# Optimization experiments

Measured on AMD Instinct MI355X. Metric: run time of the kernel, lower is better.

The kernel has to match this reference:

```python
import jax, jax.numpy as jnp
import numpy as np

P = 0.8
EPS = 1e-6


def setup_inputs() -> dict:
    key = jax.random.key(0)
    k1, k2 = jax.random.split(key)
    N, C = 8192, 2048
    logits = jax.random.normal(k1, (N, C), dtype=jnp.float32)
    labels = jax.random.randint(k2, (N,), 0, C, dtype=jnp.int64)
    return {"logits": logits, "labels": labels}


def reference(logits, labels):
    N, C = logits.shape
    # targets: one-hot class indicators, [N, C]
    targets = jax.nn.one_hot(labels, C, dtype=logits.dtype)
    # class counts (first-call behavior of the stateful module): sum over batch + 1
    class_counts = targets.sum(axis=0) + 1.0  # [C]
    # seesaw mitigation factor s[i, j] = (n_j / n_i)^p if n_i > n_j else 1
    ratio = class_counts[None, :] / class_counts[:, None]  # [C, C]
    s = jnp.where(class_counts[:, None] > class_counts[None, :], ratio ** P, 1.0)
    # stable exp
    logits = logits - logits.max(axis=-1, keepdims=True)
    e = jnp.exp(logits)  # [N, C]
    # denominator[n, i] = sum_j (1 - t[n,j]) * s[i,j] * e[n,j] + e[n,i]
    # == ((1 - t) * e) @ s.T + e  -- GEMM form of the O(N*C*C) broadcast-sum
    denom = jnp.einsum('nj,ij->ni', (1.0 - targets) * e, s) + e
    sigma = e / (denom + EPS)
    loss = (-targets * jnp.log(sigma + EPS)).sum(axis=-1)  # [N]
    return loss.mean()
```

## Files before the change

kernel.cpp:

```cpp
#include <hip/hip_runtime.h>
#include <math.h>

#define NROWS 8192
#define NCLS  2048
#define NBLK  512
#define NTHR  512
#define LOG2E 1.44269504088896340736f
#define EPS   1e-6f


__global__ __launch_bounds__(512, 4) void seesaw_rows_k(
        const float* __restrict__ logits,
        const int*   __restrict__ labels,
        float*       __restrict__ part) {
    __shared__ __align__(16) int   cnt[NCLS];
    __shared__ __align__(16) float w[NCLS];
    __shared__ float red[8];

    const int t    = threadIdx.x;
    const int lane = t & 63;
    const int wid  = t >> 6;

    const int n0 = blockIdx.x * 16 + wid * 2;
    const int n1 = n0 + 1;

    const int4* lab4 = reinterpret_cast<const int4*>(labels);
    int4 L0 = lab4[t];
    int4 L1 = lab4[t + 512];
    int4 L2 = lab4[t + 1024];
    int4 L3 = lab4[t + 1536];

    const int y0 = labels[n0];
    const int y1 = labels[n1];

    const float4* r0 = reinterpret_cast<const float4*>(logits + (size_t)n0 * NCLS);
    const float4* r1 = reinterpret_cast<const float4*>(logits + (size_t)n1 * NCLS);
    float4 va[8], vb[8];
    #pragma unroll
    for (int k = 0; k < 8; ++k) va[k] = r0[k * 64 + lane];
    #pragma unroll
    for (int k = 0; k < 8; ++k) vb[k] = r1[k * 64 + lane];

    const float ylog0 = logits[(size_t)n0 * NCLS + y0];
    const float ylog1 = logits[(size_t)n1 * NCLS + y1];

    #pragma unroll
    for (int j = t; j < NCLS; j += NTHR) cnt[j] = 0;
    asm volatile("s_waitcnt lgkmcnt(0)" ::: "memory");
    __builtin_amdgcn_s_barrier();
    asm volatile("" ::: "memory");

    atomicAdd(&cnt[L0.x], 1); atomicAdd(&cnt[L0.y], 1);
    atomicAdd(&cnt[L0.z], 1); atomicAdd(&cnt[L0.w], 1);
    atomicAdd(&cnt[L1.x], 1); atomicAdd(&cnt[L1.y], 1);
    atomicAdd(&cnt[L1.z], 1); atomicAdd(&cnt[L1.w], 1);
    atomicAdd(&cnt[L2.x], 1); atomicAdd(&cnt[L2.y], 1);
    atomicAdd(&cnt[L2.z], 1); atomicAdd(&cnt[L2.w], 1);
    atomicAdd(&cnt[L3.x], 1); atomicAdd(&cnt[L3.y], 1);
    atomicAdd(&cnt[L3.z], 1); atomicAdd(&cnt[L3.w], 1);
    asm volatile("s_waitcnt lgkmcnt(0)" ::: "memory");
    __builtin_amdgcn_s_barrier();
    asm volatile("" ::: "memory");

    #pragma unroll
    for (int j = t; j < NCLS; j += NTHR) w[j] = 0.8f * log2f((float)(cnt[j] + 1));
    asm volatile("s_waitcnt lgkmcnt(0)" ::: "memory");
    __builtin_amdgcn_s_barrier();
    asm volatile("" ::: "memory");

    const float4* wl4 = reinterpret_cast<const float4*>(w);
    const float wy0 = w[y0];
    const float wy1 = w[y1];

    float s0 = 0.0f, s1 = 0.0f;
    #pragma unroll
    for (int k = 0; k < 8; ++k) {
        float4 wv = wl4[k * 64 + lane];
        s0 += exp2f(fmaf(va[k].x, LOG2E, fminf(wv.x - wy0, 0.0f)));
        s0 += exp2f(fmaf(va[k].y, LOG2E, fminf(wv.y - wy0, 0.0f)));
        s0 += exp2f(fmaf(va[k].z, LOG2E, fminf(wv.z - wy0, 0.0f)));
        s0 += exp2f(fmaf(va[k].w, LOG2E, fminf(wv.w - wy0, 0.0f)));
        s1 += exp2f(fmaf(vb[k].x, LOG2E, fminf(wv.x - wy1, 0.0f)));
        s1 += exp2f(fmaf(vb[k].y, LOG2E, fminf(wv.y - wy1, 0.0f)));
        s1 += exp2f(fmaf(vb[k].z, LOG2E, fminf(wv.z - wy1, 0.0f)));
        s1 += exp2f(fmaf(vb[k].w, LOG2E, fminf(wv.w - wy1, 0.0f)));
    }
    #pragma unroll
    for (int off = 32; off; off >>= 1) {
        s0 += __shfl_xor(s0, off, 64);
        s1 += __shfl_xor(s1, off, 64);
    }

    if (lane == 0) {
        float ey0 = exp2f(ylog0 * LOG2E);
        float ey1 = exp2f(ylog1 * LOG2E);
        float l0 = -logf(ey0 / (s0 + EPS) + EPS);
        float l1 = -logf(ey1 / (s1 + EPS) + EPS);
        red[wid] = l0 + l1;
    }
    __syncthreads();
    if (t == 0) {
        float bs = ((red[0] + red[1]) + (red[2] + red[3])) +
                   ((red[4] + red[5]) + (red[6] + red[7]));
        part[blockIdx.x] = bs;
    }
}

__global__ __launch_bounds__(256) void finalize_k(
        const float* __restrict__ part, float* __restrict__ out) {
    const int t = threadIdx.x, lane = t & 63, wid = t >> 6;
    float s = part[t] + part[t + 256];
    #pragma unroll
    for (int off = 32; off; off >>= 1) s += __shfl_xor(s, off, 64);
    __shared__ float red[4];
    if (lane == 0) red[wid] = s;
    __syncthreads();
    if (t == 0) out[0] = ((red[0] + red[1]) + (red[2] + red[3])) / (float)NROWS;
}

extern "C" void kernel_launch(void* const* d_in, const int* in_sizes, int n_in,
                              void* d_out, int out_size, void* d_ws, size_t ws_size,
                              hipStream_t stream) {
    const float* logits = (const float*)d_in[0];
    const int*   labels = (const int*)d_in[1];
    float* out  = (float*)d_out;
    float* part = (float*)d_ws;

    seesaw_rows_k<<<NBLK, NTHR, 0, stream>>>(logits, labels, part);
    finalize_k<<<1, 256, 0, stream>>>(part, out);
}
```

Baseline: 20.44 us.

## Fuse finalize into main kernel via two-level last-block atomic reduction

Drops the separate finalize kernel. Each block publishes its partial sum, and per-group atomic counters elect a last block that reduces 32 partials; a second counter elects the final block, which writes the mean. A memset of the counters is added before the launch. The second row's loads are deferred until after the histogram phase to lower register pressure, and the exp accumulations are split into two independent chains each. This trades a kernel launch for a memset node plus atomics.

```diff
diff --git a/kernel.cpp b/kernel.cpp
--- a/kernel.cpp
+++ b/kernel.cpp
@@ -9,19 +9,24 @@
 #define EPS   1e-6f
 
 
-__global__ __launch_bounds__(512, 4) void seesaw_rows_k(
+__global__ __launch_bounds__(512, 4) void seesaw_all_k(
         const float* __restrict__ logits,
         const int*   __restrict__ labels,
-        float*       __restrict__ part) {
+        char*        __restrict__ wsb,
+        float*       __restrict__ out) {
     __shared__ __align__(16) int   cnt[NCLS];
     __shared__ __align__(16) float w[NCLS];
     __shared__ float red[8];
 
+    float* part = (float*)wsb;
+    float* gsum = (float*)(wsb + 2048);
+
     const int t    = threadIdx.x;
     const int lane = t & 63;
     const int wid  = t >> 6;
+    const int bid  = blockIdx.x;
 
-    const int n0 = blockIdx.x * 16 + wid * 2;
+    const int n0 = bid * 16 + wid * 2;
     const int n1 = n0 + 1;
 
     const int4* lab4 = reinterpret_cast<const int4*>(labels);
@@ -34,18 +39,14 @@
     const int y1 = labels[n1];
 
     const float4* r0 = reinterpret_cast<const float4*>(logits + (size_t)n0 * NCLS);
-    const float4* r1 = reinterpret_cast<const float4*>(logits + (size_t)n1 * NCLS);
-    float4 va[8], vb[8];
+    float4 va[8];
     #pragma unroll
     for (int k = 0; k < 8; ++k) va[k] = r0[k * 64 + lane];
-    #pragma unroll
-    for (int k = 0; k < 8; ++k) vb[k] = r1[k * 64 + lane];
 
     const float ylog0 = logits[(size_t)n0 * NCLS + y0];
     const float ylog1 = logits[(size_t)n1 * NCLS + y1];
 
-    #pragma unroll
-    for (int j = t; j < NCLS; j += NTHR) cnt[j] = 0;
+    reinterpret_cast<int4*>(cnt)[t] = make_int4(0, 0, 0, 0);
     asm volatile("s_waitcnt lgkmcnt(0)" ::: "memory");
     __builtin_amdgcn_s_barrier();
     asm volatile("" ::: "memory");
@@ -68,23 +69,36 @@
     __builtin_amdgcn_s_barrier();
     asm volatile("" ::: "memory");
 
+    const float4* r1 = reinterpret_cast<const float4*>(logits + (size_t)n1 * NCLS);
+    float4 vb[8];
+    #pragma unroll
+    for (int k = 0; k < 8; ++k) vb[k] = r1[k * 64 + lane];
+
     const float4* wl4 = reinterpret_cast<const float4*>(w);
     const float wy0 = w[y0];
     const float wy1 = w[y1];
 
-    float s0 = 0.0f, s1 = 0.0f;
+    float s0a = 0.0f, s0b = 0.0f;
     #pragma unroll
     for (int k = 0; k < 8; ++k) {
         float4 wv = wl4[k * 64 + lane];
-        s0 += exp2f(fmaf(va[k].x, LOG2E, fminf(wv.x - wy0, 0.0f)));
-        s0 += exp2f(fmaf(va[k].y, LOG2E, fminf(wv.y - wy0, 0.0f)));
-        s0 += exp2f(fmaf(va[k].z, LOG2E, fminf(wv.z - wy0, 0.0f)));
-        s0 += exp2f(fmaf(va[k].w, LOG2E, fminf(wv.w - wy0, 0.0f)));
-        s1 += exp2f(fmaf(vb[k].x, LOG2E, fminf(wv.x - wy1, 0.0f)));
-        s1 += exp2f(fmaf(vb[k].y, LOG2E, fminf(wv.y - wy1, 0.0f)));
-        s1 += exp2f(fmaf(vb[k].z, LOG2E, fminf(wv.z - wy1, 0.0f)));
-        s1 += exp2f(fmaf(vb[k].w, LOG2E, fminf(wv.w - wy1, 0.0f)));
+        s0a += exp2f(fmaf(va[k].x, LOG2E, fminf(wv.x - wy0, 0.0f)));
+        s0b += exp2f(fmaf(va[k].y, LOG2E, fminf(wv.y - wy0, 0.0f)));
+        s0a += exp2f(fmaf(va[k].z, LOG2E, fminf(wv.z - wy0, 0.0f)));
+        s0b += exp2f(fmaf(va[k].w, LOG2E, fminf(wv.w - wy0, 0.0f)));
     }
+    float s1a = 0.0f, s1b = 0.0f;
+    #pragma unroll
+    for (int k = 0; k < 8; ++k) {
+        float4 wv = wl4[k * 64 + lane];
+        s1a += exp2f(fmaf(vb[k].x, LOG2E, fminf(wv.x - wy1, 0.0f)));
+        s1b += exp2f(fmaf(vb[k].y, LOG2E, fminf(wv.y - wy1, 0.0f)));
+        s1a += exp2f(fmaf(vb[k].z, LOG2E, fminf(wv.z - wy1, 0.0f)));
+        s1b += exp2f(fmaf(vb[k].w, LOG2E, fminf(wv.w - wy1, 0.0f)));
+    }
+
+    float s0 = s0a + s0b;
+    float s1 = s1a + s1b;
     #pragma unroll
     for (int off = 32; off; off >>= 1) {
         s0 += __shfl_xor(s0, off, 64);
@@ -99,23 +113,51 @@
         red[wid] = l0 + l1;
     }
     __syncthreads();
+
     if (t == 0) {
         float bs = ((red[0] + red[1]) + (red[2] + red[3])) +
                    ((red[4] + red[5]) + (red[6] + red[7]));
-        part[blockIdx.x] = bs;
+        __hip_atomic_store(&part[bid], bs, __ATOMIC_RELAXED,
+                           __HIP_MEMORY_SCOPE_AGENT);
     }
-}
-
-__global__ __launch_bounds__(256) void finalize_k(
-        const float* __restrict__ part, float* __restrict__ out) {
-    const int t = threadIdx.x, lane = t & 63, wid = t >> 6;
-    float s = part[t] + part[t + 256];
-    #pragma unroll
-    for (int off = 32; off; off >>= 1) s += __shfl_xor(s, off, 64);
-    __shared__ float red[4];
-    if (lane == 0) red[wid] = s;
-    __syncthreads();
-    if (t == 0) out[0] = ((red[0] + red[1]) + (red[2] + red[3])) / (float)NROWS;
+    if (t < 64) {
+        const int g = bid >> 5;
+        int rc = -1;
+        if (t == 0) {
+            unsigned* gc = (unsigned*)(wsb + 4096 + (size_t)g * 64);
+            rc = (int)__hip_atomic_fetch_add(gc, 1u, __ATOMIC_ACQ_REL,
+                                             __HIP_MEMORY_SCOPE_AGENT);
+        }
+        rc = __shfl(rc, 0, 64);
+        if (rc == 31) {
+            __threadfence();
+            float p = 0.0f;
+            if (t < 32)
+                p = __hip_atomic_load(&part[g * 32 + t], __ATOMIC_RELAXED,
+                                      __HIP_MEMORY_SCOPE_AGENT);
+            #pragma unroll
+            for (int off = 16; off; off >>= 1) p += __shfl_xor(p, off, 32);
+            int rc2 = -1;
+            if (t == 0) {
+                __hip_atomic_store(&gsum[g], p, __ATOMIC_RELAXED,
+                                   __HIP_MEMORY_SCOPE_AGENT);
+                unsigned* fc = (unsigned*)(wsb + 5120);
+                rc2 = (int)__hip_atomic_fetch_add(fc, 1u, __ATOMIC_ACQ_REL,
+                                                  __HIP_MEMORY_SCOPE_AGENT);
+            }
+            rc2 = __shfl(rc2, 0, 64);
+            if (rc2 == 15) {
+                __threadfence();
+                float q = 0.0f;
+                if (t < 16)
+                    q = __hip_atomic_load(&gsum[t], __ATOMIC_RELAXED,
+                                          __HIP_MEMORY_SCOPE_AGENT);
+                #pragma unroll
+                for (int off = 8; off; off >>= 1) q += __shfl_xor(q, off, 32);
+                if (t == 0) out[0] = q / (float)NROWS;
+            }
+        }
+    }
 }
 
 extern "C" void kernel_launch(void* const* d_in, const int* in_sizes, int n_in,
@@ -123,9 +165,9 @@
                               hipStream_t stream) {
     const float* logits = (const float*)d_in[0];
     const int*   labels = (const int*)d_in[1];
-    float* out  = (float*)d_out;
-    float* part = (float*)d_ws;
+    float* out = (float*)d_out;
+    char*  wsb = (char*)d_ws;
 
-    seesaw_rows_k<<<NBLK, NTHR, 0, stream>>>(logits, labels, part);
-    finalize_k<<<1, 256, 0, stream>>>(part, out);
+    hipMemsetAsync(wsb + 4096, 0, 1088, stream);
+    seesaw_all_k<<<NBLK, NTHR, 0, stream>>>(logits, labels, wsb, out);
 }
```

Result: slower. 37.12 us (+81.6%).

## Process one row per wave and double the block count

Applied to the files above, without the earlier changes.

Each wave now handles one row instead of two, so the grid doubles to 1024 blocks and the launch bound rises to 6 blocks per CU, lowering register pressure to allow more resident waves. The sum is split into two accumulators for more instruction-level parallelism, the count zeroing uses one vector store, and the finalize kernel reads partials as float4. The cost is that each block rebuilds the full label histogram, so that redundant per-block work doubles.

```diff
diff --git a/kernel.cpp b/kernel.cpp
--- a/kernel.cpp
+++ b/kernel.cpp
@@ -3,13 +3,13 @@
 
 #define NROWS 8192
 #define NCLS  2048
-#define NBLK  512
+#define NBLK  1024
 #define NTHR  512
 #define LOG2E 1.44269504088896340736f
 #define EPS   1e-6f
 
 
-__global__ __launch_bounds__(512, 4) void seesaw_rows_k(
+__global__ __launch_bounds__(512, 6) void seesaw_rows_k(
         const float* __restrict__ logits,
         const int*   __restrict__ labels,
         float*       __restrict__ part) {
@@ -20,9 +20,7 @@
     const int t    = threadIdx.x;
     const int lane = t & 63;
     const int wid  = t >> 6;
-
-    const int n0 = blockIdx.x * 16 + wid * 2;
-    const int n1 = n0 + 1;
+    const int n    = blockIdx.x * 8 + wid;
 
     const int4* lab4 = reinterpret_cast<const int4*>(labels);
     int4 L0 = lab4[t];
@@ -30,22 +28,16 @@
     int4 L2 = lab4[t + 1024];
     int4 L3 = lab4[t + 1536];
 
-    const int y0 = labels[n0];
-    const int y1 = labels[n1];
+    const int y = labels[n];
 
-    const float4* r0 = reinterpret_cast<const float4*>(logits + (size_t)n0 * NCLS);
-    const float4* r1 = reinterpret_cast<const float4*>(logits + (size_t)n1 * NCLS);
-    float4 va[8], vb[8];
+    const float4* r0 = reinterpret_cast<const float4*>(logits + (size_t)n * NCLS);
+    float4 v[8];
     #pragma unroll
-    for (int k = 0; k < 8; ++k) va[k] = r0[k * 64 + lane];
-    #pragma unroll
-    for (int k = 0; k < 8; ++k) vb[k] = r1[k * 64 + lane];
+    for (int k = 0; k < 8; ++k) v[k] = r0[k * 64 + lane];
 
-    const float ylog0 = logits[(size_t)n0 * NCLS + y0];
-    const float ylog1 = logits[(size_t)n1 * NCLS + y1];
+    const float ylogit = logits[(size_t)n * NCLS + y];
 
-    #pragma unroll
-    for (int j = t; j < NCLS; j += NTHR) cnt[j] = 0;
+    reinterpret_cast<int4*>(cnt)[t] = make_int4(0, 0, 0, 0);
     asm volatile("s_waitcnt lgkmcnt(0)" ::: "memory");
     __builtin_amdgcn_s_barrier();
     asm volatile("" ::: "memory");
@@ -69,34 +61,24 @@
     asm volatile("" ::: "memory");
 
     const float4* wl4 = reinterpret_cast<const float4*>(w);
-    const float wy0 = w[y0];
-    const float wy1 = w[y1];
+    const float wy = w[y];
 
-    float s0 = 0.0f, s1 = 0.0f;
+    float sa = 0.0f, sb = 0.0f;
     #pragma unroll
     for (int k = 0; k < 8; ++k) {
         float4 wv = wl4[k * 64 + lane];
-        s0 += exp2f(fmaf(va[k].x, LOG2E, fminf(wv.x - wy0, 0.0f)));
-        s0 += exp2f(fmaf(va[k].y, LOG2E, fminf(wv.y - wy0, 0.0f)));
-        s0 += exp2f(fmaf(va[k].z, LOG2E, fminf(wv.z - wy0, 0.0f)));
-        s0 += exp2f(fmaf(va[k].w, LOG2E, fminf(wv.w - wy0, 0.0f)));
-        s1 += exp2f(fmaf(vb[k].x, LOG2E, fminf(wv.x - wy1, 0.0f)));
-        s1 += exp2f(fmaf(vb[k].y, LOG2E, fminf(wv.y - wy1, 0.0f)));
-        s1 += exp2f(fmaf(vb[k].z, LOG2E, fminf(wv.z - wy1, 0.0f)));
-        s1 += exp2f(fmaf(vb[k].w, LOG2E, fminf(wv.w - wy1, 0.0f)));
+        sa += exp2f(fmaf(v[k].x, LOG2E, fminf(wv.x - wy, 0.0f)));
+        sb += exp2f(fmaf(v[k].y, LOG2E, fminf(wv.y - wy, 0.0f)));
+        sa += exp2f(fmaf(v[k].z, LOG2E, fminf(wv.z - wy, 0.0f)));
+        sb += exp2f(fmaf(v[k].w, LOG2E, fminf(wv.w - wy, 0.0f)));
     }
+    float s = sa + sb;
     #pragma unroll
-    for (int off = 32; off; off >>= 1) {
-        s0 += __shfl_xor(s0, off, 64);
-        s1 += __shfl_xor(s1, off, 64);
-    }
+    for (int off = 32; off; off >>= 1) s += __shfl_xor(s, off, 64);
 
     if (lane == 0) {
-        float ey0 = exp2f(ylog0 * LOG2E);
-        float ey1 = exp2f(ylog1 * LOG2E);
-        float l0 = -logf(ey0 / (s0 + EPS) + EPS);
-        float l1 = -logf(ey1 / (s1 + EPS) + EPS);
-        red[wid] = l0 + l1;
+        float ey = exp2f(ylogit * LOG2E);
+        red[wid] = -logf(ey / (s + EPS) + EPS);
     }
     __syncthreads();
     if (t == 0) {
@@ -109,7 +91,9 @@
 __global__ __launch_bounds__(256) void finalize_k(
         const float* __restrict__ part, float* __restrict__ out) {
     const int t = threadIdx.x, lane = t & 63, wid = t >> 6;
-    float s = part[t] + part[t + 256];
+    const float4* p4 = reinterpret_cast<const float4*>(part);
+    float4 v = p4[t];
+    float s = (v.x + v.y) + (v.z + v.w);
     #pragma unroll
     for (int off = 32; off; off >>= 1) s += __shfl_xor(s, off, 64);
     __shared__ float red[4];
```

Result: faster. 18.80 us (-8.0%).
